# Kernel tuning notes

Hardware: AMD Instinct MI355X
Metric: run time of the kernel (lower is better)

## Reference

```python
import jax, jax.numpy as jnp
import numpy as np

N_Q = 4  # n_qubits == hidden_dim


def _qgate(z, phi):
    # Quantum circuit closed form: all gates are single-qubit RX, so the state is a
    # product state. Wires 0,1 get RX(z[:,w]) encoding then trainable RX(phi[w]);
    # wires >=2 get only trainable RX(phi[w]). <PauliZ> after RX(theta)|0> = cos(theta).
    B = z.shape[0]
    ang01 = z[:, :2] + phi[:2]                                  # [B, 2]
    ang_rest = jnp.broadcast_to(phi[2:], (B, N_Q - 2))          # [B, N_Q-2]
    return jnp.cos(jnp.concatenate([ang01, ang_rest], axis=1))  # [B, N_Q]


def setup_inputs() -> dict:
    key = jax.random.key(0)
    ks = jax.random.split(key, 13)
    T, B, D, H = 512, 256, 256, N_Q
    s = 0.1
    inp = {"inputs": jax.random.normal(ks[0], (T, B, D), dtype=jnp.float32)}
    for j, n in enumerate(["f", "i", "u", "o"]):
        inp["W" + n] = jax.random.normal(ks[1 + 3 * j], (H, D + H), dtype=jnp.float32) * s
        inp["b" + n] = jax.random.normal(ks[2 + 3 * j], (H,), dtype=jnp.float32) * s
        inp["phi_" + n] = jax.random.normal(ks[3 + 3 * j], (H,), dtype=jnp.float32) * s
    return inp


def reference(inputs, Wf, bf, phi_f, Wi, bi, phi_i, Wu, bu, phi_u, Wo, bo, phi_o):
    B = inputs.shape[1]
    H = Wf.shape[0]

    def step(carry, x):
        hx, cx = carry
        c = jnp.concatenate([x, hx], axis=1)                     # [B, D+H]
        f = jax.nn.sigmoid(_qgate(c @ Wf.T + bf, phi_f))
        i = jax.nn.sigmoid(_qgate(c @ Wi.T + bi, phi_i))
        g = jnp.tanh(_qgate(c @ Wu.T + bu, phi_u))
        o = jax.nn.sigmoid(_qgate(c @ Wo.T + bo, phi_o))
        cx_new = f * cx + i * g
        hx_new = o * jnp.tanh(cx_new)
        return (hx_new, cx_new), hx_new

    h0 = jnp.zeros((B, H), inputs.dtype)
    c0 = jnp.zeros((B, H), inputs.dtype)
    (hx, cx), outputs = jax.lax.scan(step, (h0, c0), inputs)
    return outputs, hx, cx
```

## Files before the change

### kernel.cpp

```cpp
#include <hip/hip_runtime.h>
#include <math.h>

#define TT 512
#define BB 256
#define DD 256
#define ROWS (TT * BB)
#define INV2PI 0.15915494309189535f
#define CHUNK 32
#define WARM 24
#define NCH (TT / CHUNK)

typedef float v2f __attribute__((ext_vector_type(2)));
typedef float v4f __attribute__((ext_vector_type(4)));

__device__ __forceinline__ v2f pkfma(v2f a, v2f b, v2f c) {
    return __builtin_elementwise_fma(a, b, c);
}
__device__ __forceinline__ v2f cos2(v2f a) {
    v2f r;
    r.x = __builtin_amdgcn_cosf(a.x);
    r.y = __builtin_amdgcn_cosf(a.y);
    return r;
}
__device__ __forceinline__ v2f sig2(v2f x) {
    v2f u = x * x;
    v2f p = pkfma(u, (v2f)(-2.1081349e-4f), (v2f)(2.0833333e-3f));
    p = pkfma(u, p, (v2f)(-2.0833333e-2f));
    p = pkfma(u, p, (v2f)(0.25f));
    return pkfma(x, p, (v2f)(0.5f));
}
__device__ __forceinline__ v2f tanh2(v2f x) {
    v2f u = x * x;
    v2f n = pkfma(u + (v2f)(105.0f), u, (v2f)(945.0f));
    v2f d = pkfma(pkfma(u, (v2f)(15.0f), (v2f)(420.0f)), u, (v2f)(945.0f));
    v2f r;
    r.x = __builtin_amdgcn_rcpf(d.x);
    r.y = __builtin_amdgcn_rcpf(d.y);
    return x * n * r;
}

__device__ __forceinline__ float reduce8(float p[8], int lane) {
    const bool b0 = lane & 1;
#pragma unroll
    for (int k = 0; k < 4; ++k) {
        float send = b0 ? p[k] : p[k + 4];
        float q = __shfl_xor(send, 1, 64);
        p[k] = (b0 ? p[k + 4] : p[k]) + q;
    }
    const bool b1 = lane & 2;
#pragma unroll
    for (int k = 0; k < 2; ++k) {
        float send = b1 ? p[k] : p[k + 2];
        float q = __shfl_xor(send, 2, 64);
        p[k] = (b1 ? p[k + 2] : p[k]) + q;
    }
    const bool b2 = lane & 4;
    {
        float send = b2 ? p[0] : p[1];
        float q = __shfl_xor(send, 4, 64);
        p[0] = (b2 ? p[1] : p[0]) + q;
    }
    p[0] += __shfl_xor(p[0], 8, 64);
    p[0] += __shfl_xor(p[0], 16, 64);
    p[0] += __shfl_xor(p[0], 32, 64);
    return p[0];
}

__global__ __launch_bounds__(256) void qlstm_gemm(
    const float* __restrict__ x,
    const float* __restrict__ Wf, const float* __restrict__ bf, const float* __restrict__ pf,
    const float* __restrict__ Wi, const float* __restrict__ bi, const float* __restrict__ pi,
    const float* __restrict__ Wu, const float* __restrict__ bu, const float* __restrict__ pu,
    const float* __restrict__ Wo, const float* __restrict__ bo, const float* __restrict__ po,
    float* __restrict__ Z, float* __restrict__ out) {
    __shared__ float hcf[TT * 8];
    __shared__ float hob[TT * 2];
    const int tid = threadIdx.x;
    const float* Ws[4] = {Wf, Wi, Wu, Wo};
    const float* Bs[4] = {bf, bi, bu, bo};
    const float* Ps[4] = {pf, pi, pu, po};

    float l2fc[2], Scc[2], occ[2], ricc[2];
#pragma unroll
    for (int w = 0; w < 2; ++w) {
        const int q = w + 2;
        float fv = 1.0f / (1.0f + expf(-cosf(Ps[0][q])));
        float iv = 1.0f / (1.0f + expf(-cosf(Ps[1][q])));
        float gv = tanhf(cosf(Ps[2][q]));
        float ov = 1.0f / (1.0f + expf(-cosf(Ps[3][q])));
        l2fc[w] = log2f(fv);
        Scc[w] = iv * gv;
        occ[w] = ov;
        ricc[w] = 1.0f / (1.0f - fv);
    }
    float bb[8];
#pragma unroll
    for (int g = 0; g < 4; ++g)
#pragma unroll
        for (int wire = 0; wire < 2; ++wire) bb[g * 2 + wire] = Bs[g][wire] + Ps[g][wire];

    for (int t = tid; t < TT; t += 256) {
        float h2 = occ[0] * tanhf(Scc[0] * (1.0f - exp2f((float)t * l2fc[0])) * ricc[0]);
        float h3 = occ[1] * tanhf(Scc[1] * (1.0f - exp2f((float)t * l2fc[1])) * ricc[1]);
        float ho2 = occ[0] * tanhf(Scc[0] * (1.0f - exp2f((float)(t + 1) * l2fc[0])) * ricc[0]);
        float ho3 = occ[1] * tanhf(Scc[1] * (1.0f - exp2f((float)(t + 1) * l2fc[1])) * ricc[1]);
#pragma unroll
        for (int g = 0; g < 4; ++g)
#pragma unroll
            for (int wire = 0; wire < 2; ++wire)
                hcf[t * 8 + g * 2 + wire] =
                    (bb[g * 2 + wire] + h2 * Ws[g][wire * 260 + 258] + h3 * Ws[g][wire * 260 + 259]) * INV2PI;
        hob[t * 2] = ho2;
        hob[t * 2 + 1] = ho3;
    }
    __syncthreads();

    const int lane = tid & 63;
    const int wid = (blockIdx.x * 256 + tid) >> 6;
    float4 wv[8];
#pragma unroll
    for (int g = 0; g < 4; ++g)
#pragma unroll
        for (int wire = 0; wire < 2; ++wire)
            wv[g * 2 + wire] = *(const float4*)(Ws[g] + wire * 260 + 4 * lane);
    const int v = ((lane & 1) << 2) | (lane & 2) | ((lane >> 2) & 1);

#pragma unroll
    for (int k = 0; k < 16; k += 4) {
        v4f xv[4];
#pragma unroll
        for (int j = 0; j < 4; ++j) {
            const int r = wid + (k + j) * 8192;
            xv[j] = *(const v4f*)(x + (size_t)r * DD + 4 * lane);
        }
        float s[4];
#pragma unroll
        for (int j = 0; j < 4; ++j) {
            float p[8];
#pragma unroll
            for (int m = 0; m < 8; ++m)
                p[m] = xv[j].x * wv[m].x + xv[j].y * wv[m].y + xv[j].z * wv[m].z + xv[j].w * wv[m].w;
            s[j] = reduce8(p, lane);
        }
        if (lane < 8) {
#pragma unroll
            for (int j = 0; j < 4; ++j) {
                const int r = wid + (k + j) * 8192;
                Z[(size_t)r * 8 + v] = s[j] * INV2PI + hcf[((r >> 8) << 3) + v];
            }
        } else if (lane < 12) {
            const int r = wid + (k + lane - 8) * 8192;
            *(float2*)(out + (size_t)r * 4 + 2) = *(const float2*)&hob[(r >> 8) * 2];
        }
    }
}

__global__ __launch_bounds__(64) void qlstm_scan(
    const float* __restrict__ Z,
    const float* __restrict__ Wf, const float* __restrict__ pf,
    const float* __restrict__ Wi, const float* __restrict__ pi,
    const float* __restrict__ Wu, const float* __restrict__ pu,
    const float* __restrict__ Wo, const float* __restrict__ po,
    float* __restrict__ out) {
    const int tid = threadIdx.x;
    const int chunk = blockIdx.x >> 2;
    const int b = (blockIdx.x & 3) * 64 + tid;
    const float* Ws[4] = {Wf, Wi, Wu, Wo};
    const float* Ps[4] = {pf, pi, pu, po};

    float cd[2], hd[2];
#pragma unroll
    for (int w = 0; w < 2; ++w) {
        const int q = w + 2;
        float fv = 1.0f / (1.0f + expf(-cosf(Ps[0][q])));
        float iv = 1.0f / (1.0f + expf(-cosf(Ps[1][q])));
        float gv = tanhf(cosf(Ps[2][q]));
        float ov = 1.0f / (1.0f + expf(-cosf(Ps[3][q])));
        float l2f = log2f(fv);
        float S = iv * gv;
        float ric = 1.0f / (1.0f - fv);
        cd[w] = S * (1.0f - exp2f(512.0f * l2f)) * ric;
        hd[w] = ov * tanhf(cd[w]);
    }

    v2f wa[4], wb[4];
#pragma unroll
    for (int g = 0; g < 4; ++g) {
        wa[g].x = Ws[g][256] * INV2PI;
        wa[g].y = Ws[g][260 + 256] * INV2PI;
        wb[g].x = Ws[g][257] * INV2PI;
        wb[g].y = Ws[g][260 + 257] * INV2PI;
    }

    const int t0 = chunk * CHUNK;
    const int tw = (t0 - WARM > 0) ? (t0 - WARM) : 0;
    const int len = t0 + CHUNK - tw;

    v2f h = (v2f)(0.0f), c = (v2f)(0.0f);
    const float* Zb = Z + (size_t)b * 8;
    float* outp = out + (size_t)b * 4;
    v4f zbuf[8][2];
#pragma unroll
    for (int s = 0; s < 8; ++s) {
        zbuf[s][0] = *(const v4f*)(Zb + (size_t)(tw + s) * 2048);
        zbuf[s][1] = *(const v4f*)(Zb + (size_t)(tw + s) * 2048 + 4);
    }

#pragma unroll 8
    for (int s = 0; s < len; ++s) {
        const int t = tw + s;
        const int slot = s & 7;
        v4f zA = zbuf[slot][0], zB = zbuf[slot][1];
        if (s + 8 < len) {
            zbuf[slot][0] = *(const v4f*)(Zb + (size_t)(t + 8) * 2048);
            zbuf[slot][1] = *(const v4f*)(Zb + (size_t)(t + 8) * 2048 + 4);
        }
        v2f zf = {zA.x, zA.y}, zi = {zA.z, zA.w}, zu = {zB.x, zB.y}, zo = {zB.z, zB.w};
        v2f h0s = (v2f)(h.x), h1s = (v2f)(h.y);
        v2f af = pkfma(h0s, wa[0], pkfma(h1s, wb[0], zf));
        v2f ai = pkfma(h0s, wa[1], pkfma(h1s, wb[1], zi));
        v2f au = pkfma(h0s, wa[2], pkfma(h1s, wb[2], zu));
        v2f ao = pkfma(h0s, wa[3], pkfma(h1s, wb[3], zo));
        v2f f = sig2(cos2(af));
        v2f i = sig2(cos2(ai));
        v2f g = tanh2(cos2(au));
        v2f o = sig2(cos2(ao));
        c = pkfma(f, c, i * g);
        v2f th = tanh2(c);
        h = o * th;
        if (t >= t0)
            *(v2f*)(outp + (size_t)t * (BB * 4)) = h;
    }

    if (chunk == NCH - 1) {
        *(float4*)(out + (size_t)TT * BB * 4 + (size_t)b * 4) =
            make_float4(h.x, h.y, hd[0], hd[1]);
        *(float4*)(out + (size_t)TT * BB * 4 + (size_t)BB * 4 + (size_t)b * 4) =
            make_float4(c.x, c.y, cd[0], cd[1]);
    }
}

extern "C" void kernel_launch(void* const* d_in, const int* in_sizes, int n_in,
                              void* d_out, int out_size, void* d_ws, size_t ws_size,
                              hipStream_t stream) {
    (void)in_sizes; (void)n_in; (void)out_size; (void)ws_size;
    const float* x  = (const float*)d_in[0];
    const float* Wf = (const float*)d_in[1];
    const float* bf = (const float*)d_in[2];
    const float* pf = (const float*)d_in[3];
    const float* Wi = (const float*)d_in[4];
    const float* bi = (const float*)d_in[5];
    const float* pi = (const float*)d_in[6];
    const float* Wu = (const float*)d_in[7];
    const float* bu = (const float*)d_in[8];
    const float* pu = (const float*)d_in[9];
    const float* Wo = (const float*)d_in[10];
    const float* bo = (const float*)d_in[11];
    const float* po = (const float*)d_in[12];
    float* out = (float*)d_out;
    float* Z = (float*)d_ws;

    qlstm_gemm<<<2048, 256, 0, stream>>>(x, Wf, bf, pf, Wi, bi, pi, Wu, bu, pu,
                                         Wo, bo, po, Z, out);
    qlstm_scan<<<NCH * 4, 64, 0, stream>>>(Z, Wf, pf, Wi, pi, Wu, pu, Wo, po, out);
}
```

Baseline: 234.0 us.

## Split per-timestep setup into separate kernel and double-buffer x loads in GEMM

Before this change, each of the 2048 GEMM blocks recomputed the per-timestep constant tables (hcf, hob) in shared memory with transcendentals and a barrier. That work now runs once in a single-block setup kernel that writes the tables to workspace, and the GEMM reads them from global memory. The GEMM loop also prefetches the next group of x rows while computing the current one, to hide load latency. This adds an extra kernel launch, extra workspace use, and more register pressure from the double buffer.

```diff
diff --git a/kernel.cpp b/kernel.cpp
--- a/kernel.cpp
+++ b/kernel.cpp
@@ -4,7 +4,6 @@
 #define TT 512
 #define BB 256
 #define DD 256
-#define ROWS (TT * BB)
 #define INV2PI 0.15915494309189535f
 #define CHUNK 32
 #define WARM 24
@@ -66,15 +65,12 @@
     return p[0];
 }
 
-__global__ __launch_bounds__(256) void qlstm_gemm(
-    const float* __restrict__ x,
+__global__ __launch_bounds__(256) void qlstm_setup(
     const float* __restrict__ Wf, const float* __restrict__ bf, const float* __restrict__ pf,
     const float* __restrict__ Wi, const float* __restrict__ bi, const float* __restrict__ pi,
     const float* __restrict__ Wu, const float* __restrict__ bu, const float* __restrict__ pu,
     const float* __restrict__ Wo, const float* __restrict__ bo, const float* __restrict__ po,
-    float* __restrict__ Z, float* __restrict__ out) {
-    __shared__ float hcf[TT * 8];
-    __shared__ float hob[TT * 2];
+    float* __restrict__ hcf, float* __restrict__ hob) {
     const int tid = threadIdx.x;
     const float* Ws[4] = {Wf, Wi, Wu, Wo};
     const float* Bs[4] = {bf, bi, bu, bo};
@@ -113,10 +109,20 @@
         hob[t * 2] = ho2;
         hob[t * 2 + 1] = ho3;
     }
-    __syncthreads();
-
+}
+
+__global__ __launch_bounds__(256) void qlstm_gemm(
+    const float* __restrict__ x,
+    const float* __restrict__ Wf, const float* __restrict__ Wi,
+    const float* __restrict__ Wu, const float* __restrict__ Wo,
+    const float* __restrict__ hcf, const float* __restrict__ hob,
+    float* __restrict__ Z, float* __restrict__ out) {
+    const int tid = threadIdx.x;
     const int lane = tid & 63;
     const int wid = (blockIdx.x * 256 + tid) >> 6;
+    const int tbase = wid >> 8;
+    const float* Ws[4] = {Wf, Wi, Wu, Wo};
+
     float4 wv[8];
 #pragma unroll
     for (int g = 0; g < 4; ++g)
@@ -125,32 +131,42 @@
             wv[g * 2 + wire] = *(const float4*)(Ws[g] + wire * 260 + 4 * lane);
     const int v = ((lane & 1) << 2) | (lane & 2) | ((lane >> 2) & 1);
 
+    v4f xcur[4], xnxt[4];
+#pragma unroll
+    for (int j = 0; j < 4; ++j)
+        xcur[j] = *(const v4f*)(x + (size_t)(wid + j * 8192) * DD + 4 * lane);
+
 #pragma unroll
     for (int k = 0; k < 16; k += 4) {
-        v4f xv[4];
-#pragma unroll
-        for (int j = 0; j < 4; ++j) {
-            const int r = wid + (k + j) * 8192;
-            xv[j] = *(const v4f*)(x + (size_t)r * DD + 4 * lane);
-        }
-        float s[4];
+        float hv[4];
+        float2 hb;
+        if (lane < 8) {
+#pragma unroll
+            for (int j = 0; j < 4; ++j) hv[j] = hcf[(tbase + (k + j) * 32) * 8 + v];
+        } else if (lane < 12) {
+            hb = *(const float2*)(hob + (tbase + (k + lane - 8) * 32) * 2);
+        }
+        if (k < 12) {
+#pragma unroll
+            for (int j = 0; j < 4; ++j)
+                xnxt[j] = *(const v4f*)(x + (size_t)(wid + (k + 4 + j) * 8192) * DD + 4 * lane);
+        }
 #pragma unroll
         for (int j = 0; j < 4; ++j) {
             float p[8];
 #pragma unroll
             for (int m = 0; m < 8; ++m)
-                p[m] = xv[j].x * wv[m].x + xv[j].y * wv[m].y + xv[j].z * wv[m].z + xv[j].w * wv[m].w;
-            s[j] = reduce8(p, lane);
-        }
-        if (lane < 8) {
-#pragma unroll
-            for (int j = 0; j < 4; ++j) {
-                const int r = wid + (k + j) * 8192;
-                Z[(size_t)r * 8 + v] = s[j] * INV2PI + hcf[((r >> 8) << 3) + v];
-            }
-        } else if (lane < 12) {
-            const int r = wid + (k + lane - 8) * 8192;
-            *(float2*)(out + (size_t)r * 4 + 2) = *(const float2*)&hob[(r >> 8) * 2];
+                p[m] = xcur[j].x * wv[m].x + xcur[j].y * wv[m].y + xcur[j].z * wv[m].z +
+                       xcur[j].w * wv[m].w;
+            float s = reduce8(p, lane);
+            if (lane < 8)
+                Z[(size_t)(wid + (k + j) * 8192) * 8 + v] = s * INV2PI + hv[j];
+        }
+        if (lane >= 8 && lane < 12)
+            *(float2*)(out + (size_t)(wid + (k + lane - 8) * 8192) * 4 + 2) = hb;
+        if (k < 12) {
+#pragma unroll
+            for (int j = 0; j < 4; ++j) xcur[j] = xnxt[j];
         }
     }
 }
@@ -259,8 +275,11 @@
     const float* po = (const float*)d_in[12];
     float* out = (float*)d_out;
     float* Z = (float*)d_ws;
-
-    qlstm_gemm<<<2048, 256, 0, stream>>>(x, Wf, bf, pf, Wi, bi, pi, Wu, bu, pu,
-                                         Wo, bo, po, Z, out);
+    float* hcf = Z + (size_t)TT * BB * 8;
+    float* hob = hcf + (size_t)TT * 8;
+
+    qlstm_setup<<<1, 256, 0, stream>>>(Wf, bf, pf, Wi, bi, pi, Wu, bu, pu,
+                                       Wo, bo, po, hcf, hob);
+    qlstm_gemm<<<2048, 256, 0, stream>>>(x, Wf, Wi, Wu, Wo, hcf, hob, Z, out);
     qlstm_scan<<<NCH * 4, 64, 0, stream>>>(Z, Wf, pf, Wi, pi, Wu, pu, Wo, po, out);
 }
```

Result: no change. 237.0 us (+1.3%).
